# Performance work log

Hardware: AMD Instinct MI355X
Metric: run time of the kernel (lower is better)

The kernel has to match this reference:

```python
import jax, jax.numpy as jnp
import numpy as np

D = 1024      # in_features
H = 8         # heads per branch (head_num // 2)
DH = (D // 2) // H  # 64
OUT = 1024

def _split_heads(x, B, S):
    # [B, S, D/2] -> [B, H, S, DH]
    return x.reshape(B, S, H, DH).transpose(0, 2, 1, 3)

def _attn(q, k, v):
    # q,k,v: [B, H, S, DH]
    scores = jnp.einsum('bhqd,bhkd->bhqk', q, k) / jnp.sqrt(jnp.float32(DH))
    a = jax.nn.softmax(scores, axis=-1)
    return jnp.einsum('bhqk,bhkd->bhqd', a, v)

def setup_inputs() -> dict:
    key = jax.random.key(0)
    ks = jax.random.split(key, 16)
    B, S = 2, 2048
    d2 = D // 2
    sc = lambda fan_in: 1.0 / np.sqrt(fan_in)
    inp = {
        'f1': jax.random.normal(ks[0], (B, S, D), jnp.float32),
        'f2': jax.random.normal(ks[1], (B, S, D), jnp.float32),
    }
    names = ['qs', 'ks', 'vs', 'qc', 'kc', 'vc']
    for i, n in enumerate(names):
        inp['W' + n] = jax.random.uniform(ks[2 + i], (d2, D), jnp.float32, -sc(D), sc(D))
        inp['b' + n] = jax.random.uniform(ks[8 + i], (d2,), jnp.float32, -sc(D), sc(D))
    inp['Wo'] = jax.random.uniform(ks[14], (OUT, 2 * D), jnp.float32, -sc(2 * D), sc(2 * D))
    inp['bo'] = jax.random.uniform(ks[15], (OUT,), jnp.float32, -sc(2 * D), sc(2 * D))
    return inp

def reference(f1, f2, Wqs, bqs, Wks, bks, Wvs, bvs, Wqc, bqc, Wkc, bkc, Wvc, bvc, Wo, bo):
    B, S, _ = f1.shape
    lin = lambda x, W, b: jax.nn.relu(x @ W.T + b)
    qs = lin(f1, Wqs, bqs); ks_ = lin(f1, Wks, bks); vs = lin(f1, Wvs, bvs)
    qc = lin(f1, Wqc, bqc); kc = lin(f2, Wkc, bkc); vc = lin(f2, Wvc, bvc)
    ys = _attn(_split_heads(qs, B, S), _split_heads(ks_, B, S), _split_heads(vs, B, S))
    yc = _attn(_split_heads(qc, B, S), _split_heads(kc, B, S), _split_heads(vc, B, S))
    merge = lambda y: y.transpose(0, 2, 1, 3).reshape(B, S, D // 2)
    # reshape_to_batches followed by reshape_from_batches on vs/vc is identity
    y = jnp.concatenate([merge(ys), merge(yc), vs, vc], axis=-1)  # [B, S, 2D]
    return jax.nn.relu(y @ Wo.T + bo)
```

## Files before the change

kernel.cpp:

```cpp
#include <hip/hip_runtime.h>
#include <hip/hip_bf16.h>

using bf16 = __hip_bfloat16;
typedef __attribute__((ext_vector_type(8))) short bf16x8;
typedef __attribute__((ext_vector_type(4))) short s16x4;
typedef __attribute__((ext_vector_type(4))) float f32x4;
typedef __attribute__((ext_vector_type(16))) float f32x16;
typedef __attribute__((ext_vector_type(4))) unsigned int u32x4;

#define MTOT 4096

__device__ __forceinline__ f32x4 fzero() {
    f32x4 z = {0.f, 0.f, 0.f, 0.f};
    return z;
}
__device__ __forceinline__ f32x16 fzero16() {
    f32x16 z = {0.f,0.f,0.f,0.f,0.f,0.f,0.f,0.f,0.f,0.f,0.f,0.f,0.f,0.f,0.f,0.f};
    return z;
}

__device__ __forceinline__ f32x4 mfma16(bf16x8 a, bf16x8 b, f32x4 c) {
    return __builtin_amdgcn_mfma_f32_16x16x32_bf16(a, b, c, 0, 0, 0);
}
__device__ __forceinline__ f32x16 mfma32(bf16x8 a, bf16x8 b, f32x16 c) {
    return __builtin_amdgcn_mfma_f32_32x32x16_bf16(a, b, c, 0, 0, 0);
}

__device__ __forceinline__ float exp2_raw(float x) {
    float r;
    asm("v_exp_f32 %0, %1" : "=v"(r) : "v"(x));
    return r;
}

typedef const __attribute__((address_space(1))) unsigned int* gas_ptr;
typedef __attribute__((address_space(3))) unsigned int* las_ptr;
__device__ __forceinline__ void async_copy16(const bf16* g, bf16* l) {
    __builtin_amdgcn_global_load_lds((gas_ptr)(const void*)g, (las_ptr)(void*)l, 16, 0, 0);
}

__device__ __forceinline__ bf16x8 load8(const bf16* p) {
    return *(const bf16x8*)p;
}
__device__ __forceinline__ bf16x8 load8(const float* p) {
    float4 a = *(const float4*)p;
    float4 b = *(const float4*)(p + 4);
    bf16 t[8];
    t[0] = __float2bfloat16(a.x); t[1] = __float2bfloat16(a.y);
    t[2] = __float2bfloat16(a.z); t[3] = __float2bfloat16(a.w);
    t[4] = __float2bfloat16(b.x); t[5] = __float2bfloat16(b.y);
    t[6] = __float2bfloat16(b.z); t[7] = __float2bfloat16(b.w);
    return *(const bf16x8*)t;
}

__device__ __forceinline__ void store_out(bf16* C, size_t idx, float v) {
    C[idx] = __float2bfloat16(v);
}
__device__ __forceinline__ void store_out(float* C, size_t idx, float v) {
    C[idx] = v;
}
__device__ __forceinline__ short bf16_bits(float v) {
    return __builtin_bit_cast(short, __float2bfloat16(v));
}

__global__ void MultiHeadSelfCrossAttention_7834020348638_kernel(float* out, int n) {
    int i = blockIdx.x * blockDim.x + threadIdx.x;
    if (i < n) out[i] = 0.25f;
}

struct CvtArgs {
    const float* src[9];
    bf16* dst[9];
    int start8[10];
};
__global__ void cvt_kernel(CvtArgs a) {
    int t = blockIdx.x * blockDim.x + threadIdx.x;
    if (t >= a.start8[9]) return;
    int seg = 0;
#pragma unroll
    for (int s = 1; s < 9; s++) seg += (t >= a.start8[s]) ? 1 : 0;
    int off = t - a.start8[seg];
    *(bf16x8*)(a.dst[seg] + (size_t)off * 8) = load8(a.src[seg] + (size_t)off * 8);
}

template <int BM, int BN, typename TC>
__device__ __forceinline__ void gemm_fast(
    const bf16* __restrict__ A, int lda,
    const bf16* __restrict__ Bt, int ldb,
    const float* __restrict__ bias,
    TC* __restrict__ C, int ldc,
    int K, int m0, int n0, bf16* __restrict__ VTW)
{
    constexpr int MI  = BM / 32;
    constexpr int NI  = BN / 32;
    constexpr int ACH = BM * 64 / 8 / 256;
    constexpr int BCH = BN * 64 / 8 / 256;

    __shared__ bf16 As[BM * 64];
    __shared__ bf16 Bs[BN * 64];

    const int tid  = threadIdx.x;
    const int lane = tid & 63;
    const int l15  = lane & 15, quad = lane >> 4;
    const int wave = tid >> 6;
    const int wr   = wave >> 1, wc = wave & 1;

    f32x4 acc[MI][NI];
#pragma unroll
    for (int mi = 0; mi < MI; mi++)
#pragma unroll
        for (int ni = 0; ni < NI; ni++)
            acc[mi][ni] = fzero();

    for (int k0 = 0; k0 < K; k0 += 64) {
        __syncthreads();
#pragma unroll
        for (int i = 0; i < ACH; i++) {
            int idx = i * 256 + tid;
            int r   = idx >> 3;
            int sl  = (idx & 7) ^ (r & 7);
            async_copy16(A + (size_t)(m0 + r) * lda + k0 + sl * 8, &As[idx * 8]);
        }
#pragma unroll
        for (int i = 0; i < BCH; i++) {
            int idx = i * 256 + tid;
            int r   = idx >> 3;
            int sl  = (idx & 7) ^ (r & 7);
            async_copy16(Bt + (size_t)(n0 + r) * ldb + k0 + sl * 8, &Bs[idx * 8]);
        }
        __syncthreads();

#pragma unroll
        for (int ks = 0; ks < 2; ks++) {
            bf16x8 af[MI], bfr[NI];
#pragma unroll
            for (int mi = 0; mi < MI; mi++) {
                int row = wr * (BM / 2) + mi * 16 + l15;
                af[mi] = *(const bf16x8*)&As[row * 64 + (((ks * 4 + quad) ^ (row & 7)) * 8)];
            }
#pragma unroll
            for (int ni = 0; ni < NI; ni++) {
                int row = wc * (BN / 2) + ni * 16 + l15;
                bfr[ni] = *(const bf16x8*)&Bs[row * 64 + (((ks * 4 + quad) ^ (row & 7)) * 8)];
            }
#pragma unroll
            for (int mi = 0; mi < MI; mi++)
#pragma unroll
                for (int ni = 0; ni < NI; ni++)
                    acc[mi][ni] = mfma16(af[mi], bfr[ni], acc[mi][ni]);
        }
    }

#pragma unroll
    for (int ni = 0; ni < NI; ni++) {
        int col = n0 + wc * (BN / 2) + ni * 16 + l15;
        float bb = bias[col];
#pragma unroll
        for (int mi = 0; mi < MI; mi++) {
            float v0 = fmaxf(acc[mi][ni][0] + bb, 0.f);
            float v1 = fmaxf(acc[mi][ni][1] + bb, 0.f);
            float v2 = fmaxf(acc[mi][ni][2] + bb, 0.f);
            float v3 = fmaxf(acc[mi][ni][3] + bb, 0.f);
            int row0 = m0 + wr * (BM / 2) + mi * 16 + quad * 4;
            store_out(C, (size_t)(row0 + 0) * ldc + col, v0);
            store_out(C, (size_t)(row0 + 1) * ldc + col, v1);
            store_out(C, (size_t)(row0 + 2) * ldc + col, v2);
            store_out(C, (size_t)(row0 + 3) * ldc + col, v3);
            if (VTW) {
                int h = col >> 6, d = col & 63;
                int s = row0 & 2047, b2 = row0 >> 11;
                short tv[4] = {bf16_bits(v0), bf16_bits(v1), bf16_bits(v2), bf16_bits(v3)};
                *(s16x4*)&VTW[((size_t)(b2 * 8 + h)) * 64 * 2048 + (size_t)d * 2048 + s] =
                    *(const s16x4*)tv;
            }
        }
    }
}

template <int BN, typename TA, typename TB, typename TC>
__device__ __forceinline__ void gemm_reg(
    const TA* __restrict__ A, int lda,
    const TB* __restrict__ Bt, int ldb,
    const float* __restrict__ bias,
    TC* __restrict__ C, int ldc,
    int K, int m0, int n0)
{
    constexpr int NI  = BN / 32;
    constexpr int BCH = BN * 4 / 256;

    __shared__ bf16 As[128 * 32];
    __shared__ bf16 Bs[BN * 32];

    const int tid  = threadIdx.x;
    const int lane = tid & 63;
    const int l15  = lane & 15, quad = lane >> 4;
    const int wave = tid >> 6;
    const int wr   = wave >> 1, wc = wave & 1;

    f32x4 acc[4][NI];
#pragma unroll
    for (int mi = 0; mi < 4; mi++)
#pragma unroll
        for (int ni = 0; ni < NI; ni++)
            acc[mi][ni] = fzero();

    for (int k0 = 0; k0 < K; k0 += 32) {
        bf16x8 ra[2], rb[BCH];
#pragma unroll
        for (int i = 0; i < 2; i++) {
            int idx = i * 256 + tid;
            ra[i] = load8(A + (size_t)(m0 + (idx >> 2)) * lda + k0 + (idx & 3) * 8);
        }
#pragma unroll
        for (int i = 0; i < BCH; i++) {
            int idx = i * 256 + tid;
            rb[i] = load8(Bt + (size_t)(n0 + (idx >> 2)) * ldb + k0 + (idx & 3) * 8);
        }
        __syncthreads();
#pragma unroll
        for (int i = 0; i < 2; i++)
            *(bf16x8*)&As[(i * 256 + tid) * 8] = ra[i];
#pragma unroll
        for (int i = 0; i < BCH; i++)
            *(bf16x8*)&Bs[(i * 256 + tid) * 8] = rb[i];
        __syncthreads();

        bf16x8 af[4], bfr[NI];
#pragma unroll
        for (int mi = 0; mi < 4; mi++)
            af[mi] = *(const bf16x8*)&As[(wr * 64 + mi * 16 + l15) * 32 + quad * 8];
#pragma unroll
        for (int ni = 0; ni < NI; ni++)
            bfr[ni] = *(const bf16x8*)&Bs[(wc * (BN / 2) + ni * 16 + l15) * 32 + quad * 8];
#pragma unroll
        for (int mi = 0; mi < 4; mi++)
#pragma unroll
            for (int ni = 0; ni < NI; ni++)
                acc[mi][ni] = mfma16(af[mi], bfr[ni], acc[mi][ni]);
    }

#pragma unroll
    for (int ni = 0; ni < NI; ni++) {
        int col = n0 + wc * (BN / 2) + ni * 16 + l15;
        float bb = bias[col];
#pragma unroll
        for (int mi = 0; mi < 4; mi++) {
#pragma unroll
            for (int r = 0; r < 4; r++) {
                int row = m0 + wr * 64 + mi * 16 + quad * 4 + r;
                store_out(C, (size_t)row * ldc + col, fmaxf(acc[mi][ni][r] + bb, 0.f));
            }
        }
    }
}

__global__ __launch_bounds__(256, 4) void proj_fast(
    const bf16* __restrict__ F1, const bf16* __restrict__ F2,
    const bf16* __restrict__ Wb,
    const float* __restrict__ bqs, const float* __restrict__ bks,
    const float* __restrict__ bvs, const float* __restrict__ bqc,
    const float* __restrict__ bkc, const float* __restrict__ bvc,
    bf16* __restrict__ Y, bf16* Qs, bf16* Ks, bf16* Qc, bf16* Kc,
    bf16* __restrict__ VT)
{
    const int lid   = blockIdx.x;
    const int xcd   = lid & 7, slot = lid >> 3;
    const int panel = xcd * 24 + (slot >> 2);
    const int xb    = slot & 3;
    const int g     = panel >> 5, yb = panel & 31;
    const int m0 = yb * 128, n0 = xb * 128;

    const bf16* X; const float* bi; bf16* C; int ldc;
    switch (g) {
        case 0:  X = F1; bi = bqs; C = Qs;       ldc = 512;  break;
        case 1:  X = F1; bi = bks; C = Ks;       ldc = 512;  break;
        case 2:  X = F1; bi = bvs; C = Y + 1024; ldc = 2048; break;
        case 3:  X = F1; bi = bqc; C = Qc;       ldc = 512;  break;
        case 4:  X = F2; bi = bkc; C = Kc;       ldc = 512;  break;
        default: X = F2; bi = bvc; C = Y + 1536; ldc = 2048; break;
    }
    bf16* vtw = nullptr;
    if (VT && (g == 2 || g == 5))
        vtw = VT + (size_t)(g == 5 ? 2 * 8 * 64 * 2048 : 0);
    gemm_fast<128, 128, bf16>(X, 1024, Wb + (size_t)g * 512 * 1024, 1024, bi, C, ldc,
                              1024, m0, n0, vtw);
}

__global__ __launch_bounds__(256, 4) void out_fast(
    const bf16* __restrict__ Y, const bf16* __restrict__ WoB,
    const float* __restrict__ bo, float* __restrict__ out)
{
    const int lid   = blockIdx.x;
    const int xcd   = lid & 7, slot = lid >> 3;
    const int panel = xcd * 8 + (slot >> 4);
    const int xb    = slot & 15;
    gemm_fast<64, 64, float>(Y, 2048, WoB, 2048, bo, out, 1024, 2048,
                             panel * 64, xb * 64, nullptr);
}

__global__ void proj_reg(
    const float* __restrict__ f1, const float* __restrict__ f2,
    const float* __restrict__ Wqs, const float* __restrict__ bqs,
    const float* __restrict__ Wks, const float* __restrict__ bks,
    const float* __restrict__ Wvs, const float* __restrict__ bvs,
    const float* __restrict__ Wqc, const float* __restrict__ bqc,
    const float* __restrict__ Wkc, const float* __restrict__ bkc,
    const float* __restrict__ Wvc, const float* __restrict__ bvc,
    bf16* __restrict__ Y, bf16* Qs, bf16* Ks, bf16* Qc, bf16* Kc)
{
    const int g = blockIdx.z;
    const float *X, *W, *bi; bf16* C; int ldc;
    switch (g) {
        case 0:  X = f1; W = Wqs; bi = bqs; C = Qs;       ldc = 512;  break;
        case 1:  X = f1; W = Wks; bi = bks; C = Ks;       ldc = 512;  break;
        case 2:  X = f1; W = Wvs; bi = bvs; C = Y + 1024; ldc = 2048; break;
        case 3:  X = f1; W = Wqc; bi = bqc; C = Qc;       ldc = 512;  break;
        case 4:  X = f2; W = Wkc; bi = bkc; C = Kc;       ldc = 512;  break;
        default: X = f2; W = Wvc; bi = bvc; C = Y + 1536; ldc = 2048; break;
    }
    gemm_reg<128>(X, 1024, W, 1024, bi, C, ldc, 1024, blockIdx.y * 128, blockIdx.x * 128);
}

__global__ void out_reg(const bf16* __restrict__ Y, const float* __restrict__ Wo,
                        const float* __restrict__ bo, float* __restrict__ out)
{
    gemm_reg<64>(Y, 2048, Wo, 2048, bo, out, 1024, 2048, blockIdx.y * 128, blockIdx.x * 64);
}

__global__ __launch_bounds__(256, 4) void attn2_kernel(
    const bf16* __restrict__ Qsb, const bf16* __restrict__ Ksb,
    const bf16* __restrict__ Qcb, const bf16* __restrict__ Kcb,
    const bf16* __restrict__ VT, bf16* __restrict__ Y)
{
    __shared__ bf16 SMEM[4][64 * 64];

    const int tid  = threadIdx.x;
    const int lane = tid & 63;
    const int l31  = lane & 31;
    const int hi   = lane >> 5;
    const int wave = tid >> 6;

    const int lid   = blockIdx.x + 16 * blockIdx.y + 256 * blockIdx.z;
    const int xcd   = lid & 7, slot = lid >> 3;
    const int combo = xcd + 8 * (slot >> 4);
    const int qt    = slot & 15;
    const int bh    = combo & 15, br = combo >> 4;
    const int b = bh >> 3, h = bh & 7;

    const bf16* Qb = (br ? Qcb : Qsb) + (size_t)b * 2048 * 512 + h * 64;
    const bf16* Kb = (br ? Kcb : Ksb) + (size_t)b * 2048 * 512 + h * 64;
    const bf16* Vt = VT + ((size_t)((br * 2 + b) * 8 + h)) * 64 * 2048;
    bf16*       Ob = Y + (size_t)b * 2048 * 2048 + br * 512 + h * 64;
    const int q0 = qt * 128;

    bf16* QP = &SMEM[0][0];

#pragma unroll
    for (int i = 0; i < 4; i++) {
        int idx = i * 256 + tid;
        int r = idx >> 3, c0 = (idx & 7) * 8;
        *(bf16x8*)&QP[r * 72 + c0] = *(const bf16x8*)&Qb[(size_t)(q0 + r) * 512 + c0];
    }
    __syncthreads();

    bf16x8 qf[4];
#pragma unroll
    for (int kq = 0; kq < 4; kq++)
        qf[kq] = *(const bf16x8*)&QP[(wave * 32 + l31) * 72 + kq * 16 + hi * 8];
    __syncthreads();

#pragma unroll
    for (int i = 0; i < 2; i++) {
        int idx = i * 256 + tid;
        int r = idx >> 3, sl = (idx & 7) ^ (r & 7);
        async_copy16(Kb + (size_t)r * 512 + sl * 8, &SMEM[0][idx * 8]);
    }
#pragma unroll
    for (int i = 0; i < 2; i++) {
        int idx = i * 256 + tid;
        int r = idx >> 3, sl = (idx & 7) ^ (r & 7);
        async_copy16(Vt + (size_t)r * 2048 + sl * 8, &SMEM[1][idx * 8]);
    }
    __syncthreads();

    const short one_bits = (l31 == 0) ? (short)0x3F80 : (short)0;
    bf16x8 onesA;
#pragma unroll
    for (int j = 0; j < 8; j++) onesA[j] = one_bits;

    f32x16 o[2], ol;
    o[0] = fzero16(); o[1] = fzero16(); ol = fzero16();

    const float C1 = 0.18033688011112043f;
    const float C2 = -5.7707801635558535f;

    for (int jt = 0; jt < 32; jt++) {
        const int cur = jt & 1;
        const bf16* Kc = &SMEM[cur * 2][0];
        const bf16* Vc = &SMEM[cur * 2 + 1][0];

        if (jt < 31) {
            const size_t s0n = (size_t)(jt + 1) * 64;
            bf16* Kn = &SMEM[(cur ^ 1) * 2][0];
            bf16* Vn = &SMEM[(cur ^ 1) * 2 + 1][0];
#pragma unroll
            for (int i = 0; i < 2; i++) {
                int idx = i * 256 + tid;
                int r = idx >> 3, sl = (idx & 7) ^ (r & 7);
                async_copy16(Kb + (s0n + r) * 512 + sl * 8, &Kn[idx * 8]);
            }
#pragma unroll
            for (int i = 0; i < 2; i++) {
                int idx = i * 256 + tid;
                int r = idx >> 3, sl = (idx & 7) ^ (r & 7);
                async_copy16(Vt + (size_t)r * 2048 + s0n + sl * 8, &Vn[idx * 8]);
            }
        }

        f32x16 st[2];
        st[0] = fzero16(); st[1] = fzero16();
        __builtin_amdgcn_s_setprio(1);
#pragma unroll
        for (int t = 0; t < 2; t++)
#pragma unroll
            for (int kq = 0; kq < 4; kq++) {
                bf16x8 kf = *(const bf16x8*)&Kc[(t * 32 + l31) * 64
                               + (((kq * 2 + hi) ^ (l31 & 7)) * 8)];
                st[t] = mfma32(kf, qf[kq], st[t]);
            }
        __builtin_amdgcn_s_setprio(0);

        unsigned int pk[2][4][2];
#pragma unroll
        for (int t = 0; t < 2; t++)
#pragma unroll
            for (int g = 0; g < 4; g++) {
                float e0 = exp2_raw(fmaf(st[t][4 * g + 0], C1, C2));
                float e1 = exp2_raw(fmaf(st[t][4 * g + 1], C1, C2));
                float e2 = exp2_raw(fmaf(st[t][4 * g + 2], C1, C2));
                float e3 = exp2_raw(fmaf(st[t][4 * g + 3], C1, C2));
                asm("v_cvt_pk_bf16_f32 %0, %1, %2"
                    : "=v"(pk[t][g][0]) : "v"(e0), "v"(e1));
                asm("v_cvt_pk_bf16_f32 %0, %1, %2"
                    : "=v"(pk[t][g][1]) : "v"(e2), "v"(e3));
            }

        __builtin_amdgcn_s_setprio(1);
#pragma unroll
        for (int kb = 0; kb < 4; kb++) {
            const int t = kb >> 1, gb = (kb & 1) * 2;
            unsigned int u0 = pk[t][gb][0],     u1 = pk[t][gb][1];
            unsigned int v0 = pk[t][gb + 1][0], v1 = pk[t][gb + 1][1];
            asm("v_permlane32_swap_b32 %0, %1" : "+v"(u0), "+v"(v0));
            asm("v_permlane32_swap_b32 %0, %1" : "+v"(u1), "+v"(v1));
            u32x4 pw; pw.x = u0; pw.y = u1; pw.z = v0; pw.w = v1;
            bf16x8 pfrag = __builtin_bit_cast(bf16x8, pw);
#pragma unroll
            for (int dt = 0; dt < 2; dt++) {
                bf16x8 vf = *(const bf16x8*)&Vc[(dt * 32 + l31) * 64
                               + (((kb * 2 + hi) ^ (l31 & 7)) * 8)];
                o[dt] = mfma32(vf, pfrag, o[dt]);
            }
            ol = mfma32(onesA, pfrag, ol);
        }
        __builtin_amdgcn_s_setprio(0);

        __syncthreads();
    }

    const float linv = 1.0f / __shfl(ol[0], l31);
#pragma unroll
    for (int dt = 0; dt < 2; dt++)
#pragma unroll
        for (int r = 0; r < 16; r++) {
            int d = dt * 32 + (r & 3) + 8 * (r >> 2) + 4 * hi;
            QP[(wave * 32 + l31) * 72 + d] = __float2bfloat16(o[dt][r] * linv);
        }
    __syncthreads();
#pragma unroll
    for (int i = 0; i < 4; i++) {
        int idx = i * 256 + tid;
        int r = idx >> 3, c0 = (idx & 7) * 8;
        *(bf16x8*)&Ob[(size_t)(q0 + r) * 2048 + c0] = *(const bf16x8*)&QP[r * 72 + c0];
    }
}

__global__ __launch_bounds__(256, 4) void attn_kernel(
    const bf16* __restrict__ Qsb, const bf16* __restrict__ Ksb,
    const bf16* __restrict__ Qcb, const bf16* __restrict__ Kcb,
    bf16* __restrict__ Y)
{
    __shared__ bf16 QP[64 * 72];
    __shared__ bf16 Ksh[64 * 72];
    __shared__ bf16 Vsh[64 * 72];

    const int tid  = threadIdx.x;
    const int lane = tid & 63;
    const int l15  = lane & 15, quad = lane >> 4;
    const int wave = tid >> 6;
    const int qt = blockIdx.x, bh = blockIdx.y, br = blockIdx.z;
    const int b = bh >> 3, h = bh & 7;

    const bf16* Qb = (br ? Qcb : Qsb) + (size_t)b * 2048 * 512 + h * 64;
    const bf16* Kb = (br ? Kcb : Ksb) + (size_t)b * 2048 * 512 + h * 64;
    const bf16* Vb = Y + (size_t)b * 2048 * 2048 + 1024 + br * 512 + h * 64;
    bf16*       Ob = Y + (size_t)b * 2048 * 2048 +        br * 512 + h * 64;
    const int q0 = qt * 64;

#pragma unroll
    for (int i = 0; i < 2; i++) {
        int idx = i * 256 + tid;
        int r = idx >> 3, c0 = (idx & 7) * 8;
        *(bf16x8*)&QP[r * 72 + c0] = *(const bf16x8*)&Qb[(size_t)(q0 + r) * 512 + c0];
    }
    __syncthreads();

    bf16x8 qf[2];
#pragma unroll
    for (int ks = 0; ks < 2; ks++)
        qf[ks] = *(const bf16x8*)&QP[(wave * 16 + l15) * 72 + ks * 32 + quad * 8];

    const short one_bits = l15 == 0 ? (short)0x3F80 : (short)0;
    bf16x8 onesf;
#pragma unroll
    for (int j = 0; j < 8; j++) onesf[j] = one_bits;

    f32x4 o[4], o_l;
    o_l = fzero();
#pragma unroll
    for (int ni = 0; ni < 4; ni++) o[ni] = fzero();

    const int kr0 = tid >> 3, kc0 = (tid & 7) * 8;
    const int kr1 = (256 + tid) >> 3;

    bf16x8 kr[2], vr[2];
    kr[0] = *(const bf16x8*)&Kb[(size_t)kr0 * 512 + kc0];
    kr[1] = *(const bf16x8*)&Kb[(size_t)kr1 * 512 + kc0];
    vr[0] = *(const bf16x8*)&Vb[(size_t)lane * 2048 + (0 * 4 + wave) * 8];
    vr[1] = *(const bf16x8*)&Vb[(size_t)lane * 2048 + (1 * 4 + wave) * 8];

    for (int jt = 0; jt < 32; jt++) {
        __syncthreads();
        *(bf16x8*)&Ksh[kr0 * 72 + kc0] = kr[0];
        *(bf16x8*)&Ksh[kr1 * 72 + kc0] = kr[1];
#pragma unroll
        for (int i = 0; i < 2; i++) {
            int cg = i * 4 + wave;
            const bf16* e = (const bf16*)&vr[i];
#pragma unroll
            for (int j = 0; j < 8; j++)
                Vsh[(cg * 8 + j) * 72 + lane] = e[j];
        }
        __syncthreads();

        {
            const int s0n = (jt < 31) ? (jt + 1) * 64 : 31 * 64;
            kr[0] = *(const bf16x8*)&Kb[(size_t)(s0n + kr0) * 512 + kc0];
            kr[1] = *(const bf16x8*)&Kb[(size_t)(s0n + kr1) * 512 + kc0];
            vr[0] = *(const bf16x8*)&Vb[(size_t)(s0n + lane) * 2048 + (0 * 4 + wave) * 8];
            vr[1] = *(const bf16x8*)&Vb[(size_t)(s0n + lane) * 2048 + (1 * 4 + wave) * 8];
        }

        f32x4 s[4];
#pragma unroll
        for (int ni = 0; ni < 4; ni++) s[ni] = fzero();
#pragma unroll
        for (int ni = 0; ni < 4; ni++)
#pragma unroll
            for (int ks = 0; ks < 2; ks++) {
                bf16x8 kf = *(const bf16x8*)&Ksh[(ni * 16 + l15) * 72 + ks * 32 + quad * 8];
                s[ni] = mfma16(qf[ks], kf, s[ni]);
            }

#pragma unroll
        for (int ni = 0; ni < 4; ni++)
#pragma unroll
            for (int r = 0; r < 4; r++) {
                float p = __expf(s[ni][r] * 0.125f - 4.0f);
                QP[(wave * 16 + quad * 4 + r) * 72 + ni * 16 + l15] = __float2bfloat16(p);
            }

#pragma unroll
        for (int ks = 0; ks < 2; ks++) {
            bf16x8 pf = *(const bf16x8*)&QP[(wave * 16 + l15) * 72 + ks * 32 + quad * 8];
#pragma unroll
            for (int ni = 0; ni < 4; ni++) {
                bf16x8 vf = *(const bf16x8*)&Vsh[(ni * 16 + l15) * 72 + ks * 32 + quad * 8];
                o[ni] = mfma16(pf, vf, o[ni]);
            }
            o_l = mfma16(pf, onesf, o_l);
        }
    }

#pragma unroll
    for (int r = 0; r < 4; r++) {
        float lsum = __shfl(o_l[r], quad << 4);
        float inv = 1.f / lsum;
        int row = q0 + wave * 16 + quad * 4 + r;
#pragma unroll
        for (int ni = 0; ni < 4; ni++)
            Ob[(size_t)row * 2048 + ni * 16 + l15] = __float2bfloat16(o[ni][r] * inv);
    }
}

extern "C" void kernel_launch(void* const* d_in, const int* in_sizes, int n_in,
                              void* d_out, int out_size, void* d_ws, size_t ws_size,
                              hipStream_t stream) {
    const size_t out_bytes = (size_t)out_size * sizeof(float);
    const size_t ws_base = ((size_t)MTOT * 2048 + 4 * (size_t)MTOT * 512) * 2;
    const size_t ws_fast = ws_base + ((size_t)2 * MTOT * 1024 + 6 * 512 * 1024 + 1024 * 2048) * 2;
    const size_t vt_elems = (size_t)2 * 2 * 8 * 64 * 2048;
    const size_t ws_fast2 = ws_fast + vt_elems * 2;

    if (n_in != 16) { hipMemsetAsync(d_out, 0x43, out_bytes, stream); return; }
    if (ws_size < ws_base) { hipMemsetAsync(d_out, 0x41, out_bytes, stream); return; }

    const float* f1  = (const float*)d_in[0];
    const float* f2  = (const float*)d_in[1];
    const float* Wqs = (const float*)d_in[2];  const float* bqs = (const float*)d_in[3];
    const float* Wks = (const float*)d_in[4];  const float* bks = (const float*)d_in[5];
    const float* Wvs = (const float*)d_in[6];  const float* bvs = (const float*)d_in[7];
    const float* Wqc = (const float*)d_in[8];  const float* bqc = (const float*)d_in[9];
    const float* Wkc = (const float*)d_in[10]; const float* bkc = (const float*)d_in[11];
    const float* Wvc = (const float*)d_in[12]; const float* bvc = (const float*)d_in[13];
    const float* Wo  = (const float*)d_in[14]; const float* bo  = (const float*)d_in[15];

    bf16* Y  = (bf16*)d_ws;
    bf16* Qs = Y  + (size_t)MTOT * 2048;
    bf16* Ks = Qs + (size_t)MTOT * 512;
    bf16* Qc = Ks + (size_t)MTOT * 512;
    bf16* Kc = Qc + (size_t)MTOT * 512;
    float* out = (float*)d_out;

    if (ws_size >= ws_fast) {
        bf16* F1  = Kc + (size_t)MTOT * 512;
        bf16* F2  = F1 + (size_t)MTOT * 1024;
        bf16* Wb  = F2 + (size_t)MTOT * 1024;
        bf16* WoB = Wb + (size_t)6 * 512 * 1024;
        bf16* VT  = WoB + (size_t)1024 * 2048;
        const bool fast2 = (ws_size >= ws_fast2);

        CvtArgs ca;
        ca.src[0] = f1;  ca.dst[0] = F1;
        ca.src[1] = f2;  ca.dst[1] = F2;
        const float* ws_[6] = {Wqs, Wks, Wvs, Wqc, Wkc, Wvc};
        for (int i = 0; i < 6; i++) {
            ca.src[2 + i] = ws_[i];
            ca.dst[2 + i] = Wb + (size_t)i * 512 * 1024;
        }
        ca.src[8] = Wo; ca.dst[8] = WoB;
        int acc8 = 0;
        const int sizes8[9] = {MTOT * 1024 / 8, MTOT * 1024 / 8,
                               512 * 1024 / 8, 512 * 1024 / 8, 512 * 1024 / 8,
                               512 * 1024 / 8, 512 * 1024 / 8, 512 * 1024 / 8,
                               1024 * 2048 / 8};
        for (int i = 0; i < 9; i++) { ca.start8[i] = acc8; acc8 += sizes8[i]; }
        ca.start8[9] = acc8;

        cvt_kernel<<<dim3((acc8 + 255) / 256), 256, 0, stream>>>(ca);
        proj_fast<<<768, 256, 0, stream>>>(
            F1, F2, Wb, bqs, bks, bvs, bqc, bkc, bvc, Y, Qs, Ks, Qc, Kc,
            fast2 ? VT : nullptr);
        if (fast2) {
            attn2_kernel<<<dim3(16, 16, 2), 256, 0, stream>>>(Qs, Ks, Qc, Kc, VT, Y);
        } else {
            attn_kernel<<<dim3(32, 16, 2), 256, 0, stream>>>(Qs, Ks, Qc, Kc, Y);
        }
        out_fast<<<1024, 256, 0, stream>>>(Y, WoB, bo, out);
    } else {
        proj_reg<<<dim3(4, 32, 6), 256, 0, stream>>>(
            f1, f2, Wqs, bqs, Wks, bks, Wvs, bvs, Wqc, bqc, Wkc, bkc, Wvc, bvc,
            Y, Qs, Ks, Qc, Kc);
        attn_kernel<<<dim3(32, 16, 2), 256, 0, stream>>>(Qs, Ks, Qc, Kc, Y);
        out_reg<<<dim3(16, 32), 256, 0, stream>>>(Y, Wo, bo, out);
    }
}
```

Before: 221.4 us.

## Stage V-transpose through LDS, enlarge attention KV tile and output GEMM tile

The projection epilogue now writes V-transpose tiles into shared memory and then emits coalesced 16-byte global stores, where before each thread did scattered 8-byte strided writes. The attention kernel processes 128 keys per iteration instead of 64, which doubles the LDS footprint and lowers launch_bounds occupancy to 2 in exchange for fewer loop iterations and barriers. The output GEMM moves from 64x64 to 128x64 tiles with half the blocks, trading parallelism for more operand reuse.

```diff
diff --git a/kernel.cpp b/kernel.cpp
--- a/kernel.cpp
+++ b/kernel.cpp
@@ -95,8 +95,9 @@
     constexpr int ACH = BM * 64 / 8 / 256;
     constexpr int BCH = BN * 64 / 8 / 256;
 
-    __shared__ bf16 As[BM * 64];
-    __shared__ bf16 Bs[BN * 64];
+    __shared__ bf16 SM[BM * 64 + BN * 64];
+    bf16* As = SM;
+    bf16* Bs = SM + BM * 64;
 
     const int tid  = threadIdx.x;
     const int lane = tid & 63;
@@ -148,6 +149,11 @@
                 for (int ni = 0; ni < NI; ni++)
                     acc[mi][ni] = mfma16(af[mi], bfr[ni], acc[mi][ni]);
         }
+    }
+
+    const bool dovt = (VTW != nullptr);
+    if constexpr (BM == 128 && BN == 128) {
+        if (dovt) __syncthreads();
     }
 
 #pragma unroll
@@ -165,12 +171,30 @@
             store_out(C, (size_t)(row0 + 1) * ldc + col, v1);
             store_out(C, (size_t)(row0 + 2) * ldc + col, v2);
             store_out(C, (size_t)(row0 + 3) * ldc + col, v3);
-            if (VTW) {
-                int h = col >> 6, d = col & 63;
-                int s = row0 & 2047, b2 = row0 >> 11;
-                short tv[4] = {bf16_bits(v0), bf16_bits(v1), bf16_bits(v2), bf16_bits(v3)};
-                *(s16x4*)&VTW[((size_t)(b2 * 8 + h)) * 64 * 2048 + (size_t)d * 2048 + s] =
-                    *(const s16x4*)tv;
+            if constexpr (BM == 128 && BN == 128) {
+                if (dovt) {
+                    int cl = wc * 64 + ni * 16 + l15;
+                    int rl0 = wr * 64 + mi * 16 + quad * 4;
+                    int rX = rl0 ^ ((cl & 7) << 3);
+                    short tv[4] = {bf16_bits(v0), bf16_bits(v1),
+                                   bf16_bits(v2), bf16_bits(v3)};
+                    *(s16x4*)&SM[cl * 128 + rX] = *(const s16x4*)tv;
+                }
+            }
+        }
+    }
+
+    if constexpr (BM == 128 && BN == 128) {
+        if (dovt) {
+            __syncthreads();
+#pragma unroll
+            for (int i = 0; i < 8; i++) {
+                int idx = i * 256 + tid;
+                int d2 = idx >> 4, j = idx & 15;
+                bf16x8 vv = *(const bf16x8*)&SM[d2 * 128 + ((j * 8) ^ ((d2 & 7) << 3))];
+                int h = (n0 + d2) >> 6, din = (n0 + d2) & 63;
+                int s = (m0 & 2047) + j * 8, b2 = m0 >> 11;
+                *(bf16x8*)&VTW[((size_t)(b2 * 8 + h) * 64 + din) * 2048 + s] = vv;
             }
         }
     }
@@ -281,8 +305,8 @@
     bf16* vtw = nullptr;
     if (VT && (g == 2 || g == 5))
         vtw = VT + (size_t)(g == 5 ? 2 * 8 * 64 * 2048 : 0);
-    gemm_fast<128, 128, bf16>(X, 1024, Wb + (size_t)g * 512 * 1024, 1024, bi, C, ldc,
-                              1024, m0, n0, vtw);
+    gemm_fast<128, 128, bf16>(X, 1024, Wb + (size_t)g * 512 * 1024, 1024, bi,
+                              C, ldc, 1024, m0, n0, vtw);
 }
 
 __global__ __launch_bounds__(256, 4) void out_fast(
@@ -291,10 +315,10 @@
 {
     const int lid   = blockIdx.x;
     const int xcd   = lid & 7, slot = lid >> 3;
-    const int panel = xcd * 8 + (slot >> 4);
+    const int panel = xcd * 4 + (slot >> 4);
     const int xb    = slot & 15;
-    gemm_fast<64, 64, float>(Y, 2048, WoB, 2048, bo, out, 1024, 2048,
-                             panel * 64, xb * 64, nullptr);
+    gemm_fast<128, 64, float>(Y, 2048, WoB, 2048, bo, out, 1024, 2048,
+                              panel * 128, xb * 64, nullptr);
 }
 
 __global__ void proj_reg(
@@ -326,12 +350,12 @@
     gemm_reg<64>(Y, 2048, Wo, 2048, bo, out, 1024, 2048, blockIdx.y * 128, blockIdx.x * 64);
 }
 
-__global__ __launch_bounds__(256, 4) void attn2_kernel(
+__global__ __launch_bounds__(256, 2) void attn2_kernel(
     const bf16* __restrict__ Qsb, const bf16* __restrict__ Ksb,
     const bf16* __restrict__ Qcb, const bf16* __restrict__ Kcb,
     const bf16* __restrict__ VT, bf16* __restrict__ Y)
 {
-    __shared__ bf16 SMEM[4][64 * 64];
+    __shared__ bf16 SMEM[4][128 * 64];
 
     const int tid  = threadIdx.x;
     const int lane = tid & 63;
@@ -369,15 +393,15 @@
     __syncthreads();
 
 #pragma unroll
-    for (int i = 0; i < 2; i++) {
+    for (int i = 0; i < 4; i++) {
         int idx = i * 256 + tid;
         int r = idx >> 3, sl = (idx & 7) ^ (r & 7);
         async_copy16(Kb + (size_t)r * 512 + sl * 8, &SMEM[0][idx * 8]);
     }
 #pragma unroll
-    for (int i = 0; i < 2; i++) {
+    for (int i = 0; i < 4; i++) {
         int idx = i * 256 + tid;
-        int r = idx >> 3, sl = (idx & 7) ^ (r & 7);
+        int r = idx >> 4, sl = (idx & 15) ^ (r & 15);
         async_copy16(Vt + (size_t)r * 2048 + sl * 8, &SMEM[1][idx * 8]);
     }
     __syncthreads();
@@ -393,34 +417,34 @@
     const float C1 = 0.18033688011112043f;
     const float C2 = -5.7707801635558535f;
 
-    for (int jt = 0; jt < 32; jt++) {
+    for (int jt = 0; jt < 16; jt++) {
         const int cur = jt & 1;
         const bf16* Kc = &SMEM[cur * 2][0];
         const bf16* Vc = &SMEM[cur * 2 + 1][0];
 
-        if (jt < 31) {
-            const size_t s0n = (size_t)(jt + 1) * 64;
+        if (jt < 15) {
+            const size_t s0n = (size_t)(jt + 1) * 128;
             bf16* Kn = &SMEM[(cur ^ 1) * 2][0];
             bf16* Vn = &SMEM[(cur ^ 1) * 2 + 1][0];
 #pragma unroll
-            for (int i = 0; i < 2; i++) {
+            for (int i = 0; i < 4; i++) {
                 int idx = i * 256 + tid;
                 int r = idx >> 3, sl = (idx & 7) ^ (r & 7);
                 async_copy16(Kb + (s0n + r) * 512 + sl * 8, &Kn[idx * 8]);
             }
 #pragma unroll
-            for (int i = 0; i < 2; i++) {
+            for (int i = 0; i < 4; i++) {
                 int idx = i * 256 + tid;
-                int r = idx >> 3, sl = (idx & 7) ^ (r & 7);
+                int r = idx >> 4, sl = (idx & 15) ^ (r & 15);
                 async_copy16(Vt + (size_t)r * 2048 + s0n + sl * 8, &Vn[idx * 8]);
             }
         }
 
-        f32x16 st[2];
-        st[0] = fzero16(); st[1] = fzero16();
+        f32x16 st[4];
+        st[0] = fzero16(); st[1] = fzero16(); st[2] = fzero16(); st[3] = fzero16();
         __builtin_amdgcn_s_setprio(1);
 #pragma unroll
-        for (int t = 0; t < 2; t++)
+        for (int t = 0; t < 4; t++)
 #pragma unroll
             for (int kq = 0; kq < 4; kq++) {
                 bf16x8 kf = *(const bf16x8*)&Kc[(t * 32 + l31) * 64
@@ -429,9 +453,9 @@
             }
         __builtin_amdgcn_s_setprio(0);
 
-        unsigned int pk[2][4][2];
-#pragma unroll
-        for (int t = 0; t < 2; t++)
+        unsigned int pk[4][4][2];
+#pragma unroll
+        for (int t = 0; t < 4; t++)
 #pragma unroll
             for (int g = 0; g < 4; g++) {
                 float e0 = exp2_raw(fmaf(st[t][4 * g + 0], C1, C2));
@@ -446,7 +470,7 @@
 
         __builtin_amdgcn_s_setprio(1);
 #pragma unroll
-        for (int kb = 0; kb < 4; kb++) {
+        for (int kb = 0; kb < 8; kb++) {
             const int t = kb >> 1, gb = (kb & 1) * 2;
             unsigned int u0 = pk[t][gb][0],     u1 = pk[t][gb][1];
             unsigned int v0 = pk[t][gb + 1][0], v1 = pk[t][gb + 1][1];
@@ -456,8 +480,8 @@
             bf16x8 pfrag = __builtin_bit_cast(bf16x8, pw);
 #pragma unroll
             for (int dt = 0; dt < 2; dt++) {
-                bf16x8 vf = *(const bf16x8*)&Vc[(dt * 32 + l31) * 64
-                               + (((kb * 2 + hi) ^ (l31 & 7)) * 8)];
+                bf16x8 vf = *(const bf16x8*)&Vc[(dt * 32 + l31) * 128
+                               + (((kb * 2 + hi) ^ (l31 & 15)) * 8)];
                 o[dt] = mfma32(vf, pfrag, o[dt]);
             }
             ol = mfma32(onesA, pfrag, ol);
@@ -665,7 +689,7 @@
         } else {
             attn_kernel<<<dim3(32, 16, 2), 256, 0, stream>>>(Qs, Ks, Qc, Kc, Y);
         }
-        out_fast<<<1024, 256, 0, stream>>>(Y, WoB, bo, out);
+        out_fast<<<512, 256, 0, stream>>>(Y, WoB, bo, out);
     } else {
         proj_reg<<<dim3(4, 32, 6), 256, 0, stream>>>(
             f1, f2, Wqs, bqs, Wks, bks, Wvs, bvs, Wqc, bqc, Wkc, bkc, Wvc, bvc,
```

Result: no change. 218.9 us (-1.1%).
